# Performance work log

Measured on AMD Instinct MI355X. Metric: run time of the kernel, lower is better.

## Reference

```python
import jax, jax.numpy as jnp
import numpy as np

D_MODEL = 64
SEQ_LEN = 9
MAX_SL = 50
TIMESTAMP = 56
ACTION_NUM = 300
BATCH = 65536


def setup_inputs() -> dict:
    key = jax.random.key(0)
    ks = jax.random.split(key, 8)
    input_actions = jax.random.randint(ks[0], (BATCH, SEQ_LEN), 0, ACTION_NUM + 1)
    emb_table = jax.random.normal(ks[1], (ACTION_NUM + 1, D_MODEL), jnp.float32) * 0.02
    emb_table = emb_table.at[0].set(0.0)  # padding_idx=0
    M_w = jax.random.normal(ks[2], (MAX_SL, D_MODEL, D_MODEL), jnp.float32) * 0.05
    M_b = jax.random.normal(ks[3], (MAX_SL, D_MODEL), jnp.float32) * 0.05
    W_w = jax.random.normal(ks[4], (TIMESTAMP, D_MODEL, D_MODEL), jnp.float32) * 0.05
    W_b = jax.random.normal(ks[5], (TIMESTAMP, D_MODEL), jnp.float32) * 0.05
    out_w = jax.random.normal(ks[6], (ACTION_NUM, D_MODEL), jnp.float32) * 0.05
    out_b = jax.random.normal(ks[7], (ACTION_NUM,), jnp.float32) * 0.05
    return {"input_actions": input_actions, "emb_table": emb_table,
            "M_w": M_w, "M_b": M_b, "W_w": W_w, "W_b": W_b,
            "out_w": out_w, "out_b": out_b}


def reference(input_actions, emb_table, M_w, M_b, W_w, W_b, out_w, out_b):
    B, S = input_actions.shape
    d = emb_table.shape[1]
    ae = emb_table[input_actions]              # [B, S, d]
    ae_t = jnp.transpose(ae, (1, 0, 2))        # [S, B, d]
    # per-timestep weight selection, matching M[min(i, len(M)-1)] and W[i % timeStamp]
    m_idx = jnp.minimum(jnp.arange(S), M_w.shape[0] - 1)
    w_idx = jnp.arange(S) % W_w.shape[0]
    Mw, Mb = M_w[m_idx], M_b[m_idx]            # [S, d, d], [S, d]
    Ww, Wb = W_w[w_idx], W_b[w_idx]

    def step(hl, xs):
        x, mw, mb, ww, wb = xs
        # torch Linear: y = x @ W.T + b
        hl = jax.nn.sigmoid(x @ mw.T + mb + hl @ ww.T + wb)
        return hl, None

    hl0 = jnp.zeros((B, d), ae.dtype)
    hl, _ = jax.lax.scan(step, hl0, (ae_t, Mw, Mb, Ww, Wb))
    return hl @ out_w.T + out_b               # [B, actionNum]
```

## Files before the change

### kernel.cpp

```cpp
#include <hip/hip_runtime.h>
#include <hip/hip_bf16.h>


#define SEQ     9
#define DMODEL  64
#define ANUM    300

#define WS_MW   0
#define WS_OW   73728
#define WS_EMB  94208
#define WS_END  113472
#define WS_BSUM_BYTES (WS_END * 2)

#define BSOFF   61440
#define HSOFF   62592
#define SLTOT   78976

typedef __attribute__((ext_vector_type(8))) short  bf16x8;
typedef __attribute__((ext_vector_type(4))) float  f32x4;

#define MFMA __builtin_amdgcn_mfma_f32_16x16x32_bf16

__device__ __forceinline__ unsigned short f2b(float f) {
    union { float f; unsigned int u; } x; x.f = f;
    unsigned int r = x.u + 0x7FFFu + ((x.u >> 16) & 1u);
    return (unsigned short)(r >> 16);
}

__device__ __forceinline__ float sigmoid_fast(float v) {
    return __builtin_amdgcn_rcpf(1.f + __expf(-v));
}

__device__ __forceinline__ void async16(const unsigned short* g, unsigned short* l) {
    __builtin_amdgcn_global_load_lds(
        (const __attribute__((address_space(1))) unsigned int*)g,
        (__attribute__((address_space(3))) unsigned int*)l, 16, 0, 0);
}

#define PP_TOTAL (73728 + 20480 + 19264 + 576)

__global__ void prepack(const float* __restrict__ Mw, const float* __restrict__ Ww,
                        const float* __restrict__ outw, const float* __restrict__ emb,
                        const float* __restrict__ Mb, const float* __restrict__ Wb,
                        unsigned short* __restrict__ wsb, float* __restrict__ bsum)
{
    int t = blockIdx.x * 256 + threadIdx.x;
    if (t < 73728) {
        int s    = t >> 13;
        int r    = t & 8191;
        int kind = r >> 12;
        int f    = r & 4095;
        int nt   = f >> 10;
        int kb   = (f >> 9) & 1;
        int lane = (f >> 3) & 63;
        int j    = f & 7;
        int nr   = nt * 16 + (lane & 15);
        int k    = kb * 32 + ((lane >> 4) << 3) + j;
        const float* src = kind ? Ww : Mw;
        wsb[WS_MW + t] = f2b(src[(s * DMODEL + nr) * DMODEL + k]);
        return;
    }
    t -= 73728;
    if (t < 20480) {
        int j    = t & 7;
        int lane = (t >> 3) & 63;
        int kb   = (t >> 9) & 1;
        int nt   = (t >> 10) & 3;
        int cc   = t >> 12;
        int col  = cc * 64 + nt * 16 + (lane & 15);
        int k    = kb * 32 + ((lane >> 4) << 3) + j;
        float v  = (col < ANUM) ? outw[col * DMODEL + k] : 0.f;
        wsb[WS_OW + t] = f2b(v);
        return;
    }
    t -= 20480;
    if (t < 19264) { wsb[WS_EMB + t] = f2b(emb[t]); return; }
    t -= 19264;
    if (t < 576)   { bsum[t] = Mb[t] + Wb[t]; }
}

__global__ __launch_bounds__(1024, 4)
void carnn_main(const int* __restrict__ acts,
                const unsigned short* __restrict__ wsb,
                const float* __restrict__ bsum,
                const float* __restrict__ outb,
                float* __restrict__ out)
{
    __shared__ __align__(16) unsigned short SL[SLTOT];

    const int tid  = threadIdx.x;
    const int lane = tid & 63;
    const int wv   = tid >> 6;
    const int lrow = lane & 15;
    const int quad = lane >> 4;

    const int brow = (blockIdx.x * 16 + wv) * 16 + lrow;
    const int rowS = brow * SEQ;

    for (int c = wv; c < 120; c += 16) {
        const int goff = (c < 8) ? (c * 512) : ((c + 8) * 512);
        async16(wsb + WS_MW + goff + lane * 8, &SL[c * 512]);
    }
    {
        const unsigned short* bs = (const unsigned short*)bsum;
        if (wv == 13) async16(bs + lane * 8,         &SL[BSOFF]);
        if (wv == 14) async16(bs + 512 + lane * 8,   &SL[BSOFF + 512]);
        if (wv == 15 && lane < 16)
                      async16(bs + 1024 + lane * 8,  &SL[BSOFF + 1024]);
    }

    const unsigned short* Eb = wsb + WS_EMB;
    int id0  = acts[rowS];
    int id1  = acts[rowS + 1];
    int idn2 = acts[rowS + 2];
    bf16x8 xc0 = *(const bf16x8*)(Eb + id0 * DMODEL + quad * 8);
    bf16x8 xc1 = *(const bf16x8*)(Eb + id0 * DMODEL + 32 + quad * 8);
    bf16x8 xn0 = *(const bf16x8*)(Eb + id1 * DMODEL + quad * 8);
    bf16x8 xn1 = *(const bf16x8*)(Eb + id1 * DMODEL + 32 + quad * 8);

    char* const SB = (char*)SL;
    const int swz    = (lrow & 7) << 4;
    const int hbyte  = HSOFF * 2 + wv * 2048 + lrow * 128;
    const int rbyte0 = hbyte + ((quad * 16) ^ swz);
    const int rbyte1 = hbyte + ((64 + quad * 16) ^ swz);

    __syncthreads();

    const float* BSf = (const float*)&SL[BSOFF];

    f32x4 xacc[4];
    #pragma unroll
    for (int nt = 0; nt < 4; ++nt) {
        const unsigned short* Mf = &SL[nt * 1024 + lane * 8];
        bf16x8 am0 = *(const bf16x8*)Mf;
        bf16x8 am1 = *(const bf16x8*)(Mf + 512);
        f32x4 a = *(const f32x4*)(BSf + nt * 16 + quad * 4);
        a = MFMA(am0, xc0, a, 0, 0, 0);
        a = MFMA(am1, xc1, a, 0, 0, 0);
        xacc[nt] = a;
    }

    #pragma unroll
    for (int s = 0; s < SEQ; ++s) {
        bf16x8 xm0, xm1;
        if (s + 2 < SEQ) {
            xm0 = *(const bf16x8*)(Eb + idn2 * DMODEL + quad * 8);
            xm1 = *(const bf16x8*)(Eb + idn2 * DMODEL + 32 + quad * 8);
            if (s + 3 < SEQ) idn2 = acts[rowS + s + 3];
        }

        bf16x8 h0, h1;
        if (s > 0) {
            h0 = *(const bf16x8*)(SB + rbyte0);
            h1 = *(const bf16x8*)(SB + rbyte1);
        }
        const unsigned short* WBh = (s == 0) ? (const unsigned short*)nullptr
                                  : (s < 8)  ? &SL[4096 + (s - 1) * 8192 + 4096]
                                             : wsb + WS_MW + 8 * 8192 + 4096;
        #pragma unroll
        for (int nt = 0; nt < 4; ++nt) {
            f32x4 acc = xacc[nt];
            if (s > 0) {
                const unsigned short* Wf = WBh + nt * 1024 + lane * 8;
                bf16x8 aw0 = *(const bf16x8*)Wf;
                bf16x8 aw1 = *(const bf16x8*)(Wf + 512);
                acc = MFMA(aw0, h0, acc, 0, 0, 0);
                acc = MFMA(aw1, h1, acc, 0, 0, 0);
            }
            unsigned int u0 = (unsigned int)f2b(sigmoid_fast(acc[0]))
                            | ((unsigned int)f2b(sigmoid_fast(acc[1])) << 16);
            unsigned int u1 = (unsigned int)f2b(sigmoid_fast(acc[2]))
                            | ((unsigned int)f2b(sigmoid_fast(acc[3])) << 16);
            *(uint2*)(SB + hbyte + ((nt * 32 + quad * 8) ^ swz)) = make_uint2(u0, u1);
        }
        asm volatile("" ::: "memory");

        if (s + 1 < SEQ) {
            const unsigned short* WBm = (s + 1 < 8) ? &SL[4096 + s * 8192]
                                                    : wsb + WS_MW + 8 * 8192;
            #pragma unroll
            for (int nt = 0; nt < 4; ++nt) {
                const unsigned short* Mf = WBm + nt * 1024 + lane * 8;
                bf16x8 am0 = *(const bf16x8*)Mf;
                bf16x8 am1 = *(const bf16x8*)(Mf + 512);
                f32x4 a = *(const f32x4*)(BSf + (s + 1) * 64 + nt * 16 + quad * 4);
                a = MFMA(am0, xn0, a, 0, 0, 0);
                a = MFMA(am1, xn1, a, 0, 0, 0);
                xacc[nt] = a;
            }
            if (s + 2 < SEQ) { xn0 = xm0; xn1 = xm1; }
        }
    }

    bf16x8 h0 = *(const bf16x8*)(SB + rbyte0);
    bf16x8 h1 = *(const bf16x8*)(SB + rbyte1);

    __syncthreads();
    for (int c = wv; c < 40; c += 16)
        async16(wsb + WS_OW + c * 512 + lane * 8, &SL[c * 512]);
    {
        const unsigned short* ob = (const unsigned short*)outb;
        if (wv == 12)               async16(ob + lane * 8,       &SL[BSOFF]);
        if (wv == 13 && lane < 11)  async16(ob + 512 + lane * 8, &SL[BSOFF + 512]);
    }
    __syncthreads();

    const float* OBf = (const float*)&SL[BSOFF];
    float* orow = out + brow * ANUM;

    #pragma unroll
    for (int t = 0; t < 19; ++t) {
        const int cc = t >> 2, nt = t & 3;
        const unsigned short* Of = &SL[cc * 4096 + nt * 1024 + lane * 8];
        bf16x8 a0 = *(const bf16x8*)Of;
        bf16x8 a1 = *(const bf16x8*)(Of + 512);
        const int col0 = cc * 64 + nt * 16 + quad * 4;

        f32x4 acc;
        if (col0 < ANUM) acc = *(const f32x4*)(OBf + col0);
        else             acc = (f32x4){0.f, 0.f, 0.f, 0.f};
        acc = MFMA(a0, h0, acc, 0, 0, 0);
        acc = MFMA(a1, h1, acc, 0, 0, 0);

        if (col0 < ANUM)
            *(f32x4*)(orow + col0) = acc;
    }
}

extern "C" void kernel_launch(void* const* d_in, const int* in_sizes, int n_in,
                              void* d_out, int out_size, void* d_ws, size_t ws_size,
                              hipStream_t stream) {
    const int*   acts = (const int*)  d_in[0];
    const float* emb  = (const float*)d_in[1];
    const float* Mw   = (const float*)d_in[2];
    const float* Mb   = (const float*)d_in[3];
    const float* Ww   = (const float*)d_in[4];
    const float* Wb   = (const float*)d_in[5];
    const float* outw = (const float*)d_in[6];
    const float* outb = (const float*)d_in[7];
    float* out = (float*)d_out;
    (void)in_sizes; (void)n_in; (void)ws_size; (void)out_size;

    unsigned short* wsb = (unsigned short*)d_ws;
    float* bsum = (float*)((char*)d_ws + WS_BSUM_BYTES);

    prepack<<<(PP_TOTAL + 255) / 256, 256, 0, stream>>>(Mw, Ww, outw, emb, Mb, Wb, wsb, bsum);
    carnn_main<<<65536 / 256, 1024, 0, stream>>>(acts, wsb, bsum, outb, out);
}
```

Baseline: 119.9 us.

## Split fused RNN kernel into recurrence and output-projection kernels

Splits the single fused kernel into an RNN kernel that writes the final hidden state as bf16 to a workspace buffer and a separate projection kernel that loads the packed output weights into LDS and computes the 300-wide logits. This removes the large output-weight LDS footprint and projection work from the recurrence kernel and lets the projection run with a different block size and occupancy. In exchange it adds a global round trip of the hidden state (8 MB) and an extra kernel launch. The path is taken only when the workspace is large enough, and the original fused kernel remains as a fallback.

```diff
diff --git a/kernel.cpp b/kernel.cpp
--- a/kernel.cpp
+++ b/kernel.cpp
@@ -11,6 +11,8 @@
 #define WS_EMB  94208
 #define WS_END  113472
 #define WS_BSUM_BYTES (WS_END * 2)
+#define WS_HG_SH  118784
+#define WS_NEED_BYTES (WS_HG_SH * 2 + 65536 * 64 * 2)
 
 #define BSOFF   61440
 #define HSOFF   62592
@@ -80,11 +82,10 @@
 }
 
 __global__ __launch_bounds__(1024, 4)
-void carnn_main(const int* __restrict__ acts,
-                const unsigned short* __restrict__ wsb,
-                const float* __restrict__ bsum,
-                const float* __restrict__ outb,
-                float* __restrict__ out)
+void carnn_rnn(const int* __restrict__ acts,
+               const unsigned short* __restrict__ wsb,
+               const float* __restrict__ bsum,
+               unsigned short* __restrict__ Hg)
 {
     __shared__ __align__(16) unsigned short SL[SLTOT];
 
@@ -148,7 +149,177 @@
             xm1 = *(const bf16x8*)(Eb + idn2 * DMODEL + 32 + quad * 8);
             if (s + 3 < SEQ) idn2 = acts[rowS + s + 3];
         }
-
+        bf16x8 h0, h1;
+        if (s > 0) {
+            h0 = *(const bf16x8*)(SB + rbyte0);
+            h1 = *(const bf16x8*)(SB + rbyte1);
+        }
+        const unsigned short* WBh = (s == 0) ? (const unsigned short*)nullptr
+                                  : (s < 8)  ? &SL[4096 + (s - 1) * 8192 + 4096]
+                                             : wsb + WS_MW + 8 * 8192 + 4096;
+        #pragma unroll
+        for (int nt = 0; nt < 4; ++nt) {
+            f32x4 acc = xacc[nt];
+            if (s > 0) {
+                const unsigned short* Wf = WBh + nt * 1024 + lane * 8;
+                bf16x8 aw0 = *(const bf16x8*)Wf;
+                bf16x8 aw1 = *(const bf16x8*)(Wf + 512);
+                acc = MFMA(aw0, h0, acc, 0, 0, 0);
+                acc = MFMA(aw1, h1, acc, 0, 0, 0);
+            }
+            unsigned int u0 = (unsigned int)f2b(sigmoid_fast(acc[0]))
+                            | ((unsigned int)f2b(sigmoid_fast(acc[1])) << 16);
+            unsigned int u1 = (unsigned int)f2b(sigmoid_fast(acc[2]))
+                            | ((unsigned int)f2b(sigmoid_fast(acc[3])) << 16);
+            if (s < 8) {
+                *(uint2*)(SB + hbyte + ((nt * 32 + quad * 8) ^ swz)) = make_uint2(u0, u1);
+            } else {
+                *(uint2*)(Hg + brow * 64 + nt * 16 + quad * 4) = make_uint2(u0, u1);
+            }
+        }
+        asm volatile("" ::: "memory");
+
+        if (s + 1 < SEQ) {
+            const unsigned short* WBm = (s + 1 < 8) ? &SL[4096 + s * 8192]
+                                                    : wsb + WS_MW + 8 * 8192;
+            #pragma unroll
+            for (int nt = 0; nt < 4; ++nt) {
+                const unsigned short* Mf = WBm + nt * 1024 + lane * 8;
+                bf16x8 am0 = *(const bf16x8*)Mf;
+                bf16x8 am1 = *(const bf16x8*)(Mf + 512);
+                f32x4 a = *(const f32x4*)(BSf + (s + 1) * 64 + nt * 16 + quad * 4);
+                a = MFMA(am0, xn0, a, 0, 0, 0);
+                a = MFMA(am1, xn1, a, 0, 0, 0);
+                xacc[nt] = a;
+            }
+            if (s + 2 < SEQ) { xn0 = xm0; xn1 = xm1; }
+        }
+    }
+}
+
+#define PB_OB 20480
+
+__global__ __launch_bounds__(512, 6)
+void carnn_proj(const unsigned short* __restrict__ wsb,
+                const float* __restrict__ outb,
+                const unsigned short* __restrict__ Hg,
+                float* __restrict__ out)
+{
+    __shared__ __align__(16) unsigned short PL[20480 + 768];
+
+    const int tid  = threadIdx.x;
+    const int lane = tid & 63;
+    const int wv   = tid >> 6;
+    const int lrow = lane & 15;
+    const int quad = lane >> 4;
+
+    const int brow = blockIdx.x * 128 + wv * 16 + lrow;
+
+    for (int c = wv; c < 40; c += 8)
+        async16(wsb + WS_OW + c * 512 + lane * 8, &PL[c * 512]);
+    {
+        const unsigned short* ob = (const unsigned short*)outb;
+        if (wv == 0)              async16(ob + lane * 8,       &PL[PB_OB]);
+        if (wv == 1 && lane < 11) async16(ob + 512 + lane * 8, &PL[PB_OB + 512]);
+    }
+
+    const unsigned short* hrow = Hg + brow * 64;
+    bf16x8 h0 = *(const bf16x8*)(hrow + quad * 8);
+    bf16x8 h1 = *(const bf16x8*)(hrow + 32 + quad * 8);
+
+    __syncthreads();
+
+    const float* OBf = (const float*)&PL[PB_OB];
+    float* orow = out + brow * ANUM;
+
+    #pragma unroll
+    for (int t = 0; t < 19; ++t) {
+        const int cc = t >> 2, nt = t & 3;
+        const unsigned short* Of = &PL[cc * 4096 + nt * 1024 + lane * 8];
+        bf16x8 a0 = *(const bf16x8*)Of;
+        bf16x8 a1 = *(const bf16x8*)(Of + 512);
+        const int col0 = cc * 64 + nt * 16 + quad * 4;
+
+        f32x4 acc;
+        if (col0 < ANUM) acc = *(const f32x4*)(OBf + col0);
+        else             acc = (f32x4){0.f, 0.f, 0.f, 0.f};
+        acc = MFMA(a0, h0, acc, 0, 0, 0);
+        acc = MFMA(a1, h1, acc, 0, 0, 0);
+
+        if (col0 < ANUM)
+            *(f32x4*)(orow + col0) = acc;
+    }
+}
+
+__global__ __launch_bounds__(1024, 4)
+void carnn_main(const int* __restrict__ acts,
+                const unsigned short* __restrict__ wsb,
+                const float* __restrict__ bsum,
+                const float* __restrict__ outb,
+                float* __restrict__ out)
+{
+    __shared__ __align__(16) unsigned short SL[SLTOT];
+
+    const int tid  = threadIdx.x;
+    const int lane = tid & 63;
+    const int wv   = tid >> 6;
+    const int lrow = lane & 15;
+    const int quad = lane >> 4;
+
+    const int brow = (blockIdx.x * 16 + wv) * 16 + lrow;
+    const int rowS = brow * SEQ;
+
+    for (int c = wv; c < 120; c += 16) {
+        const int goff = (c < 8) ? (c * 512) : ((c + 8) * 512);
+        async16(wsb + WS_MW + goff + lane * 8, &SL[c * 512]);
+    }
+    {
+        const unsigned short* bs = (const unsigned short*)bsum;
+        if (wv == 13) async16(bs + lane * 8,         &SL[BSOFF]);
+        if (wv == 14) async16(bs + 512 + lane * 8,   &SL[BSOFF + 512]);
+        if (wv == 15 && lane < 16)
+                      async16(bs + 1024 + lane * 8,  &SL[BSOFF + 1024]);
+    }
+
+    const unsigned short* Eb = wsb + WS_EMB;
+    int id0  = acts[rowS];
+    int id1  = acts[rowS + 1];
+    int idn2 = acts[rowS + 2];
+    bf16x8 xc0 = *(const bf16x8*)(Eb + id0 * DMODEL + quad * 8);
+    bf16x8 xc1 = *(const bf16x8*)(Eb + id0 * DMODEL + 32 + quad * 8);
+    bf16x8 xn0 = *(const bf16x8*)(Eb + id1 * DMODEL + quad * 8);
+    bf16x8 xn1 = *(const bf16x8*)(Eb + id1 * DMODEL + 32 + quad * 8);
+
+    char* const SB = (char*)SL;
+    const int swz    = (lrow & 7) << 4;
+    const int hbyte  = HSOFF * 2 + wv * 2048 + lrow * 128;
+    const int rbyte0 = hbyte + ((quad * 16) ^ swz);
+    const int rbyte1 = hbyte + ((64 + quad * 16) ^ swz);
+
+    __syncthreads();
+
+    const float* BSf = (const float*)&SL[BSOFF];
+
+    f32x4 xacc[4];
+    #pragma unroll
+    for (int nt = 0; nt < 4; ++nt) {
+        const unsigned short* Mf = &SL[nt * 1024 + lane * 8];
+        bf16x8 am0 = *(const bf16x8*)Mf;
+        bf16x8 am1 = *(const bf16x8*)(Mf + 512);
+        f32x4 a = *(const f32x4*)(BSf + nt * 16 + quad * 4);
+        a = MFMA(am0, xc0, a, 0, 0, 0);
+        a = MFMA(am1, xc1, a, 0, 0, 0);
+        xacc[nt] = a;
+    }
+
+    #pragma unroll
+    for (int s = 0; s < SEQ; ++s) {
+        bf16x8 xm0, xm1;
+        if (s + 2 < SEQ) {
+            xm0 = *(const bf16x8*)(Eb + idn2 * DMODEL + quad * 8);
+            xm1 = *(const bf16x8*)(Eb + idn2 * DMODEL + 32 + quad * 8);
+            if (s + 3 < SEQ) idn2 = acts[rowS + s + 3];
+        }
         bf16x8 h0, h1;
         if (s > 0) {
             h0 = *(const bf16x8*)(SB + rbyte0);
@@ -239,11 +410,18 @@
     const float* outw = (const float*)d_in[6];
     const float* outb = (const float*)d_in[7];
     float* out = (float*)d_out;
-    (void)in_sizes; (void)n_in; (void)ws_size; (void)out_size;
+    (void)in_sizes; (void)n_in; (void)out_size;
 
     unsigned short* wsb = (unsigned short*)d_ws;
     float* bsum = (float*)((char*)d_ws + WS_BSUM_BYTES);
 
     prepack<<<(PP_TOTAL + 255) / 256, 256, 0, stream>>>(Mw, Ww, outw, emb, Mb, Wb, wsb, bsum);
-    carnn_main<<<65536 / 256, 1024, 0, stream>>>(acts, wsb, bsum, outb, out);
-}
+
+    if (ws_size >= (size_t)WS_NEED_BYTES) {
+        unsigned short* Hg = wsb + WS_HG_SH;
+        carnn_rnn <<<65536 / 256, 1024, 0, stream>>>(acts, wsb, bsum, Hg);
+        carnn_proj<<<65536 / 128,  512, 0, stream>>>(wsb, outb, Hg, out);
+    } else {
+        carnn_main<<<65536 / 256, 1024, 0, stream>>>(acts, wsb, bsum, outb, out);
+    }
+}
```

Measured after the change: 126.4 us. +5.4%, slower.
